# Kernel tuning notes

Hardware: AMD Instinct MI355X
Metric: run time of the kernel (lower is better)

## Reference

```python
import jax, jax.numpy as jnp
import numpy as np

PH = 9  # pooled_height
PW = 9  # pooled_width


def _pool_roi(fm, roi):
    """Crop fm[y:y+h, x:x+w, :] and bilinear-resize to (PH, PW).
    Matches TF2 tf.image.resize (bilinear, half-pixel centers, edge-clamped).
    fm: [H, W, C] float; roi: [4] int32 = (x, y, w, h).
    """
    x, y, w, h = roi[0], roi[1], roi[2], roi[3]
    hf = h.astype(jnp.float32)
    wf = w.astype(jnp.float32)
    # half-pixel-center source coordinates within the crop
    sy = (jnp.arange(PH, dtype=jnp.float32) + 0.5) * (hf / PH) - 0.5
    sx = (jnp.arange(PW, dtype=jnp.float32) + 0.5) * (wf / PW) - 0.5
    sy = jnp.clip(sy, 0.0, hf - 1.0)
    sx = jnp.clip(sx, 0.0, wf - 1.0)
    y0 = jnp.floor(sy)
    x0 = jnp.floor(sx)
    fy = sy - y0  # [PH]
    fx = sx - x0  # [PW]
    y0i = y0.astype(jnp.int32)
    x0i = x0.astype(jnp.int32)
    y1i = jnp.minimum(y0i + 1, h - 1)
    x1i = jnp.minimum(x0i + 1, w - 1)
    # absolute indices into the full feature map
    ya0, ya1 = y + y0i, y + y1i          # [PH]
    xa0, xa1 = x + x0i, x + x1i          # [PW]
    r0 = fm[ya0]                          # [PH, W, C]
    r1 = fm[ya1]                          # [PH, W, C]
    fx_ = fx[None, :, None]
    top = r0[:, xa0, :] * (1.0 - fx_) + r0[:, xa1, :] * fx_   # [PH, PW, C]
    bot = r1[:, xa0, :] * (1.0 - fx_) + r1[:, xa1, :] * fx_   # [PH, PW, C]
    fy_ = fy[:, None, None]
    return top * (1.0 - fy_) + bot * fy_


def setup_inputs() -> dict:
    key = jax.random.key(0)
    k1, k2, k3, k4, k5 = jax.random.split(key, 5)
    B, H, W, C, R = 4, 256, 256, 256, 128
    feature_map = jax.random.normal(k1, (B, H, W, C), dtype=jnp.float32)
    # ROI sizes in [16, 128), positions so that the crop stays in-bounds
    w = jax.random.randint(k2, (B, R), 16, 128)
    h = jax.random.randint(k3, (B, R), 16, 128)
    x = jax.random.randint(k4, (B, R), 0, W - 128 + 1)
    y = jax.random.randint(k5, (B, R), 0, H - 128 + 1)
    rois = jnp.stack([x, y, w, h], axis=-1).astype(jnp.int32)  # [B, R, 4]
    return {"feature_map": feature_map, "rois": rois}


def reference(feature_map, rois):
    # vmap over ROIs within an image, then over the batch
    per_image = jax.vmap(_pool_roi, in_axes=(None, 0))   # [R, PH, PW, C]
    out = jax.vmap(per_image)(feature_map, rois)         # [B, R, PH, PW, C]
    return out
```

## Files before the change

kernel.cpp:

```cpp
#include <hip/hip_runtime.h>


#define PH 9
#define PW 9

__global__ __launch_bounds__(256) void roi_pool_kernel(
    const float* __restrict__ fm,
    const int*   __restrict__ rois,
    float*       __restrict__ out,
    int B, int H, int W, int C, int R)
{
    const int lane = threadIdx.x & 63;
    const int wave = threadIdx.x >> 6;
    const int cell = blockIdx.x * 4 + wave;
    const int ncells = B * R * PH * PW;
    if (cell >= ncells) return;

    int px = cell % PW;
    int t  = cell / PW;
    int py = t % PH;
    t /= PH;
    const int r = t % R;
    const int b = t / R;

    const int* roi = rois + (b * R + r) * 4;
    const int rx = roi[0];
    const int ry = roi[1];
    const int rw = roi[2];
    const int rh = roi[3];

    const float hf = (float)rh;
    const float wf = (float)rw;

    float sy = ((float)py + 0.5f) * (hf / (float)PH) - 0.5f;
    float sx = ((float)px + 0.5f) * (wf / (float)PW) - 0.5f;
    sy = fminf(fmaxf(sy, 0.0f), hf - 1.0f);
    sx = fminf(fmaxf(sx, 0.0f), wf - 1.0f);

    const float y0f = floorf(sy);
    const float x0f = floorf(sx);
    const float fy = sy - y0f;
    const float fx = sx - x0f;
    const int y0 = (int)y0f;
    const int x0 = (int)x0f;
    const int y1 = min(y0 + 1, rh - 1);
    const int x1 = min(x0 + 1, rw - 1);

    const long ya0 = (long)ry + y0;
    const long ya1 = (long)ry + y1;
    const long xa0 = (long)rx + x0;
    const long xa1 = (long)rx + x1;

    const long base_b = (long)b * H;
    const float4* p00 = (const float4*)(fm + ((base_b + ya0) * W + xa0) * C) + lane;
    const float4* p01 = (const float4*)(fm + ((base_b + ya0) * W + xa1) * C) + lane;
    const float4* p10 = (const float4*)(fm + ((base_b + ya1) * W + xa0) * C) + lane;
    const float4* p11 = (const float4*)(fm + ((base_b + ya1) * W + xa1) * C) + lane;

    const float4 v00 = *p00;
    const float4 v01 = *p01;
    const float4 v10 = *p10;
    const float4 v11 = *p11;

    const float gx = 1.0f - fx;
    const float gy = 1.0f - fy;

    float4 o;
    o.x = (v00.x * gx + v01.x * fx) * gy + (v10.x * gx + v11.x * fx) * fy;
    o.y = (v00.y * gx + v01.y * fx) * gy + (v10.y * gx + v11.y * fx) * fy;
    o.z = (v00.z * gx + v01.z * fx) * gy + (v10.z * gx + v11.z * fx) * fy;
    o.w = (v00.w * gx + v01.w * fx) * gy + (v10.w * gx + v11.w * fx) * fy;

    float4* po = (float4*)(out + (long)cell * C) + lane;
    *po = o;
}

extern "C" void kernel_launch(void* const* d_in, const int* in_sizes, int n_in,
                              void* d_out, int out_size, void* d_ws, size_t ws_size,
                              hipStream_t stream) {
    const float* fm   = (const float*)d_in[0];
    const int*   rois = (const int*)d_in[1];
    float*       out  = (float*)d_out;

    const int B = 4, H = 256, W = 256, C = 256, R = 128;
    const int ncells = B * R * PH * PW;
    const int blocks = (ncells + 3) / 4;

    roi_pool_kernel<<<blocks, 256, 0, stream>>>(fm, rois, out, B, H, W, C, R);
}
```

Measured before the change: 332.3 us.

## Use persistent grid-stride waves with software-prefetched loads and nontemporal stores

Replaces the one-wave-per-cell launch with a fixed grid of 2048 blocks whose waves stride over cells. Each wave issues the next cell's four gathers before blending and storing the current one, so load latency overlaps compute. The cell index is made wave-uniform with readfirstlane, and output is written with nontemporal stores to avoid polluting cache. The costs are more live registers for the double buffer and a fixed grid size that may not balance the work evenly.

```diff
diff --git a/kernel.cpp b/kernel.cpp
--- a/kernel.cpp
+++ b/kernel.cpp
@@ -3,19 +3,25 @@
 
 #define PH 9
 #define PW 9
+#define TPB 256
+#define NBLK 2048
 
-__global__ __launch_bounds__(256) void roi_pool_kernel(
-    const float* __restrict__ fm,
-    const int*   __restrict__ rois,
-    float*       __restrict__ out,
-    int B, int H, int W, int C, int R)
+typedef float f32x4 __attribute__((ext_vector_type(4)));
+
+struct Cell {
+    const f32x4* p00;
+    const f32x4* p01;
+    const f32x4* p10;
+    const f32x4* p11;
+    float fx, fy;
+};
+
+__device__ inline Cell cell_addrs(int cell, int lane,
+                                  const float* __restrict__ fm,
+                                  const int* __restrict__ rois,
+                                  int H, int W, int C, int R)
 {
-    const int lane = threadIdx.x & 63;
-    const int wave = threadIdx.x >> 6;
-    const int cell = blockIdx.x * 4 + wave;
-    const int ncells = B * R * PH * PW;
-    if (cell >= ncells) return;
-
+    Cell c;
     int px = cell % PW;
     int t  = cell / PW;
     int py = t % PH;
@@ -39,8 +45,8 @@
 
     const float y0f = floorf(sy);
     const float x0f = floorf(sx);
-    const float fy = sy - y0f;
-    const float fx = sx - x0f;
+    c.fy = sy - y0f;
+    c.fx = sx - x0f;
     const int y0 = (int)y0f;
     const int x0 = (int)x0f;
     const int y1 = min(y0 + 1, rh - 1);
@@ -52,27 +58,60 @@
     const long xa1 = (long)rx + x1;
 
     const long base_b = (long)b * H;
-    const float4* p00 = (const float4*)(fm + ((base_b + ya0) * W + xa0) * C) + lane;
-    const float4* p01 = (const float4*)(fm + ((base_b + ya0) * W + xa1) * C) + lane;
-    const float4* p10 = (const float4*)(fm + ((base_b + ya1) * W + xa0) * C) + lane;
-    const float4* p11 = (const float4*)(fm + ((base_b + ya1) * W + xa1) * C) + lane;
+    c.p00 = (const f32x4*)(fm + ((base_b + ya0) * W + xa0) * C) + lane;
+    c.p01 = (const f32x4*)(fm + ((base_b + ya0) * W + xa1) * C) + lane;
+    c.p10 = (const f32x4*)(fm + ((base_b + ya1) * W + xa0) * C) + lane;
+    c.p11 = (const f32x4*)(fm + ((base_b + ya1) * W + xa1) * C) + lane;
+    return c;
+}
 
-    const float4 v00 = *p00;
-    const float4 v01 = *p01;
-    const float4 v10 = *p10;
-    const float4 v11 = *p11;
+__global__ __launch_bounds__(TPB) void roi_pool_kernel(
+    const float* __restrict__ fm,
+    const int*   __restrict__ rois,
+    float*       __restrict__ out,
+    int B, int H, int W, int C, int R)
+{
+    const int lane   = threadIdx.x & 63;
+    const int nwaves = (NBLK * TPB) >> 6;
+    const int ncells = B * R * PH * PW;
 
-    const float gx = 1.0f - fx;
-    const float gy = 1.0f - fy;
+    int cell = (int)((blockIdx.x * TPB + threadIdx.x) >> 6);
+    cell = __builtin_amdgcn_readfirstlane(cell);
+    if (cell >= ncells) return;
 
-    float4 o;
-    o.x = (v00.x * gx + v01.x * fx) * gy + (v10.x * gx + v11.x * fx) * fy;
-    o.y = (v00.y * gx + v01.y * fx) * gy + (v10.y * gx + v11.y * fx) * fy;
-    o.z = (v00.z * gx + v01.z * fx) * gy + (v10.z * gx + v11.z * fx) * fy;
-    o.w = (v00.w * gx + v01.w * fx) * gy + (v10.w * gx + v11.w * fx) * fy;
+    Cell cur = cell_addrs(cell, lane, fm, rois, H, W, C, R);
+    f32x4 v00 = *cur.p00;
+    f32x4 v01 = *cur.p01;
+    f32x4 v10 = *cur.p10;
+    f32x4 v11 = *cur.p11;
 
-    float4* po = (float4*)(out + (long)cell * C) + lane;
-    *po = o;
+    while (true) {
+        const int nxt = cell + nwaves;
+        const bool has = (nxt < ncells);
+
+        Cell nx;
+        f32x4 w00, w01, w10, w11;
+        if (has) {
+            nx = cell_addrs(nxt, lane, fm, rois, H, W, C, R);
+            w00 = *nx.p00;
+            w01 = *nx.p01;
+            w10 = *nx.p10;
+            w11 = *nx.p11;
+        }
+
+        const float fx = cur.fx, fy = cur.fy;
+        const float gx = 1.0f - fx;
+        const float gy = 1.0f - fy;
+        f32x4 o = (v00 * gx + v01 * fx) * gy + (v10 * gx + v11 * fx) * fy;
+
+        f32x4* po = (f32x4*)(out + (long)cell * C) + lane;
+        __builtin_nontemporal_store(o, po);
+
+        if (!has) break;
+        cell = nxt;
+        cur  = nx;
+        v00 = w00; v01 = w01; v10 = w10; v11 = w11;
+    }
 }
 
 extern "C" void kernel_launch(void* const* d_in, const int* in_sizes, int n_in,
@@ -83,8 +122,6 @@
     float*       out  = (float*)d_out;
 
     const int B = 4, H = 256, W = 256, C = 256, R = 128;
-    const int ncells = B * R * PH * PW;
-    const int blocks = (ncells + 3) / 4;
 
-    roi_pool_kernel<<<blocks, 256, 0, stream>>>(fm, rois, out, B, H, W, C, R);
+    roi_pool_kernel<<<NBLK, TPB, 0, stream>>>(fm, rois, out, B, H, W, C, R);
 }
```

Result: no change. 334.8 us (median of 2 runs) (+0.7%).
